# Performance work log

Hardware: AMD Instinct MI355X
Metric: run time of the kernel (lower is better)

## Reference

```python
import jax, jax.numpy as jnp
import numpy as np

N = 100000
E = 1600000
D = 128


def setup_inputs() -> dict:
    key = jax.random.key(0)
    ks = jax.random.split(key, 6)
    x = jax.random.normal(ks[0], (N, D), dtype=jnp.float32)
    edge_row = jax.random.randint(ks[1], (E,), 0, N)
    edge_col = jax.random.randint(ks[2], (E,), 0, N)
    edge_val = jax.random.uniform(ks[3], (E,), dtype=jnp.float32)
    # Kaiming-ish init for the MLP weights
    W1 = jax.random.normal(ks[4], (D, D), dtype=jnp.float32) * (1.0 / np.sqrt(D))
    W2 = jax.random.normal(ks[5], (D, D), dtype=jnp.float32) * (1.0 / np.sqrt(D))
    b1 = jnp.zeros((D,), dtype=jnp.float32)
    b2 = jnp.zeros((D,), dtype=jnp.float32)
    eps = jnp.zeros((1,), dtype=jnp.float32)  # GIN eps, init 0
    bias = jnp.zeros((D,), dtype=jnp.float32)
    return {"x": x, "edge_row": edge_row, "edge_col": edge_col, "edge_val": edge_val,
            "W1": W1, "b1": b1, "W2": W2, "b2": b2, "eps": eps, "bias": bias}


def reference(x, edge_row, edge_col, edge_val, W1, b1, W2, b2, eps, bias):
    # sparse adj @ x : out[i] = sum_{edges (i,j)} val * x[j]
    agg = jax.ops.segment_sum(edge_val[:, None] * x[edge_col], edge_row, num_segments=N)
    h = (1.0 + eps) * x + agg                     # eps-scaled residual, [N, D]
    h = jax.nn.relu(h @ W1 + b1)                  # MLP layer 1
    h = jax.nn.relu(h @ W2 + b2)                  # MLP layer 2
    out = jax.nn.relu(h + bias)                   # bias + final relu
    return out
```

## Files before the change

kernel.cpp:

```cpp
#include <hip/hip_runtime.h>
#include <stdint.h>


static constexpr int NN = 100000;
static constexpr int NE = 1600000;
static constexpr int NB = 391;
static constexpr int EPB = 4096;
static constexpr int PB = (NE + EPB - 1) / EPB;
static constexpr int CVB = 3125;
static constexpr int SCAP = 6144;

typedef float f32x4 __attribute__((ext_vector_type(4)));
typedef short s16x8 __attribute__((ext_vector_type(8)));

__device__ __forceinline__ uint16_t f2bf(float f) {
  uint32_t u = __float_as_uint(f);
  u += 0x7fffu + ((u >> 16) & 1u);
  return (uint16_t)(u >> 16);
}
__device__ __forceinline__ float2 bf2f(uint32_t w) {
  float2 r;
  r.x = __uint_as_float(w << 16);
  r.y = __uint_as_float(w & 0xffff0000u);
  return r;
}

__device__ __forceinline__ int block_scan_inc(int v, int* wsum, int tid) {
  __syncthreads();
  int lane = tid & 63, wv = tid >> 6;
  #pragma unroll
  for (int off = 1; off < 64; off <<= 1) {
    int t = __shfl_up(v, off, 64);
    if (lane >= off) v += t;
  }
  if (lane == 63) wsum[wv] = v;
  __syncthreads();
  if (wv == 0) {
    int s = (lane < 16) ? wsum[lane] : 0;
    #pragma unroll
    for (int off = 1; off < 16; off <<= 1) {
      int t = __shfl_up(s, off, 64);
      if (lane >= off) s += t;
    }
    if (lane < 16) wsum[lane] = s;
  }
  __syncthreads();
  if (wv > 0) v += wsum[wv - 1];
  return v;
}

__global__ __launch_bounds__(1024) void k_pcvt(const float* __restrict__ x,
                                               uint32_t* __restrict__ xb,
                                               const int* __restrict__ erow,
                                               const int* __restrict__ ecol,
                                               const float* __restrict__ eval,
                                               int2* __restrict__ part,
                                               int* __restrict__ runstart) {
  int t = threadIdx.x;
  if (blockIdx.x >= PB) {
    int i = (blockIdx.x - PB) * 1024 + t;
    float4 v = ((const float4*)x)[i];
    uint2 o;
    o.x = (uint32_t)f2bf(v.x) | ((uint32_t)f2bf(v.y) << 16);
    o.y = (uint32_t)f2bf(v.z) | ((uint32_t)f2bf(v.w) << 16);
    ((uint2*)xb)[i] = o;
    return;
  }
  __shared__ int hist[NB];
  __shared__ int cur[NB];
  __shared__ int wsum[16];
  __shared__ int2 stage[EPB];
  int base = blockIdx.x * EPB;
  int cnt = min(EPB, NE - base);

  if (t < NB) hist[t] = 0;
  __syncthreads();

  int pb[4], pk[4], pv[4];
  #pragma unroll
  for (int j = 0; j < 4; ++j) {
    int i = t + j * 1024;
    pb[j] = -1;
    if (i < cnt) {
      int e = base + i;
      int r = erow[e];
      int b = r >> 8;
      pb[j] = b;
      pk[j] = ecol[e] | ((r & 255) << 17);
      pv[j] = __float_as_int(eval[e]);
      atomicAdd(&hist[b], 1);
    }
  }
  __syncthreads();

  int hv = (t < NB) ? hist[t] : 0;
  int inc = block_scan_inc(hv, wsum, t);
  if (t < NB) {
    int st = inc - hv;
    cur[t] = st;
    runstart[blockIdx.x * (NB + 1) + t] = st;
  }
  if (t == 0) runstart[blockIdx.x * (NB + 1) + NB] = cnt;
  __syncthreads();

  #pragma unroll
  for (int j = 0; j < 4; ++j) {
    if (pb[j] >= 0) {
      int off = atomicAdd(&cur[pb[j]], 1);
      stage[off] = int2{pk[j], pv[j]};
    }
  }
  __syncthreads();

  for (int i = t; i < cnt; i += 1024) part[base + i] = stage[i];
}

__global__ __launch_bounds__(1024) void k_aux(const int* __restrict__ runstart,
                                              int* __restrict__ bbase,
                                              int2* __restrict__ es_pad,
                                              const float* __restrict__ W1,
                                              const float* __restrict__ W2,
                                              uint16_t* __restrict__ wtg) {
  int t = threadIdx.x;
  if (blockIdx.x > 0) {
    int base = (blockIdx.x - 1) * 4096;
    #pragma unroll
    for (int j = 0; j < 4; ++j) {
      int idx = base + j * 1024 + t;
      int l = idx >> 14, r = idx & 16383;
      int n = r >> 7, k = r & 127;
      const float* W = l ? W2 : W1;
      wtg[idx] = f2bf(W[k * 128 + n]);
    }
    return;
  }
  __shared__ int psum[2][512];
  __shared__ int wsum[16];
  int g = t >> 9, c = t & 511;
  int acc = 0;
  if (c < NB) {
    for (int p = g; p < PB; p += 2)
      acc += runstart[p * (NB + 1) + c + 1] - runstart[p * (NB + 1) + c];
  }
  psum[g][c] = acc;
  __syncthreads();
  int v = (t < NB) ? psum[0][t] + psum[1][t] : 0;
  int inc = block_scan_inc(v, wsum, t);
  if (t < NB) bbase[t] = inc - v;
  if (t < 16) es_pad[t] = int2{0, 0};
}

__global__ __launch_bounds__(1024) void k_bucket(const int2* __restrict__ part,
                                                 const int* __restrict__ runstart,
                                                 const int* __restrict__ bbase,
                                                 int2* __restrict__ es,
                                                 int* __restrict__ rowptr) {
  __shared__ int cum[PB + 1];
  __shared__ int rbas[PB];
  __shared__ int hist[256];
  __shared__ int rps[256];
  __shared__ int cur[256];
  __shared__ int wsum[16];
  __shared__ int2 stage[SCAP];
  int b = blockIdx.x, t = threadIdx.x;
  int base_out = bbase[b];

  int len = 0;
  if (t < PB) {
    int rs = runstart[t * (NB + 1) + b];
    int re = runstart[t * (NB + 1) + b + 1];
    len = re - rs;
    rbas[t] = t * EPB + rs;
  }
  int inc1 = block_scan_inc(len, wsum, t);
  int mystart = inc1 - len;
  if (t == 1023) cum[PB] = inc1;
  if (t < 256) hist[t] = 0;
  __syncthreads();

  if (t < PB) {
    int rb = rbas[t];
    for (int i = 0; i < len; ++i) {
      int d = mystart + i;
      if (d < SCAP) stage[d] = part[rb + i];
    }
  }
  __syncthreads();

  int total = min(cum[PB], SCAP);

  for (int i = t; i < total; i += 1024)
    atomicAdd(&hist[stage[i].x >> 17], 1);
  __syncthreads();

  int hv = (t < 256) ? hist[t] : 0;
  int inc2 = block_scan_inc(hv, wsum, t);
  if (t < 256) {
    int ex = inc2 - hv;
    rps[t] = ex;
    cur[t] = ex;
  }
  __syncthreads();

  if (t < 256) {
    int row = b * 256 + t;
    if (row <= NN) rowptr[row] = base_out + rps[t];
  }

  for (int i = t; i < total; i += 1024) {
    int2 ev = stage[i];
    int rib = ev.x >> 17;
    int off = atomicAdd(&cur[rib], 1);
    es[base_out + off] = int2{ev.x & 0x1FFFF, ev.y};
  }
}

__global__ __launch_bounds__(256) void k_agg(const uint32_t* __restrict__ xb,
                                             const int2* __restrict__ es,
                                             const int* __restrict__ rowptr,
                                             const float* __restrict__ eps,
                                             uint32_t* __restrict__ hb) {
  int wid = (blockIdx.x * 256 + threadIdx.x) >> 6;
  int wave = __builtin_amdgcn_readfirstlane(wid);
  int lane = threadIdx.x & 63;
  float e = 1.0f + eps[0];
  float2 h = bf2f(xb[(size_t)wave * 64 + lane]);
  h.x *= e; h.y *= e;
  int beg = __builtin_amdgcn_readfirstlane(rowptr[wave]);
  int end = __builtin_amdgcn_readfirstlane(rowptr[wave + 1]);
  for (int k = beg; k < end; k += 8) {
    int scol[8]; float sval[8];
    #pragma unroll
    for (int j = 0; j < 8; ++j) {
      int2 ev = es[k + j];
      scol[j] = __builtin_amdgcn_readfirstlane(ev.x);
      int vb = __builtin_amdgcn_readfirstlane(ev.y);
      sval[j] = (k + j < end) ? __int_as_float(vb) : 0.0f;
    }
    uint32_t xw[8];
    #pragma unroll
    for (int j = 0; j < 8; ++j)
      xw[j] = xb[((size_t)scol[j] << 6) + lane];
    #pragma unroll
    for (int j = 0; j < 8; ++j) {
      float2 xv = bf2f(xw[j]);
      h.x = fmaf(sval[j], xv.x, h.x);
      h.y = fmaf(sval[j], xv.y, h.y);
    }
  }
  hb[(size_t)wave * 64 + lane] = (uint32_t)f2bf(h.x) | ((uint32_t)f2bf(h.y) << 16);
}

__global__ __launch_bounds__(256, 2) void k_mlp(const uint16_t* __restrict__ A,
                                                const uint16_t* __restrict__ wtg,
                                                const float* __restrict__ b1,
                                                const float* __restrict__ b2,
                                                const float* __restrict__ bias,
                                                float* __restrict__ out, int nrows) {
  __shared__ uint16_t wt[128 * 136];
  __shared__ uint16_t h1[128 * 136];
  int tid = threadIdx.x;

  const uint4* wsrc = (const uint4*)wtg;
  #pragma unroll
  for (int it = 0; it < 8; ++it) {
    int idx = tid + it * 256;
    int n = idx >> 4, kq = idx & 15;
    *(uint4*)&wt[n * 136 + kq * 8] = wsrc[idx];
  }
  __syncthreads();

  int wv = tid >> 6, l = tid & 63;
  int m16 = l & 15, qg = l >> 4;
  int r0 = blockIdx.x * 128 + wv * 32;

  int arow[2];
  #pragma unroll
  for (int mt = 0; mt < 2; ++mt) {
    int r = r0 + mt * 16 + m16;
    arow[mt] = (r < nrows) ? r : (nrows - 1);
  }

  f32x4 acc[2][8];
  #pragma unroll
  for (int mt = 0; mt < 2; ++mt)
    #pragma unroll
    for (int n0 = 0; n0 < 8; ++n0) acc[mt][n0] = f32x4{0.f, 0.f, 0.f, 0.f};

  #pragma unroll
  for (int k0 = 0; k0 < 128; k0 += 32) {
    s16x8 a[2];
    #pragma unroll
    for (int mt = 0; mt < 2; ++mt)
      a[mt] = *(const s16x8*)(A + (size_t)arow[mt] * 128 + k0 + qg * 8);
    #pragma unroll
    for (int n0 = 0; n0 < 8; ++n0) {
      s16x8 bfr = *(const s16x8*)(&wt[(n0 * 16 + m16) * 136 + k0 + qg * 8]);
      #pragma unroll
      for (int mt = 0; mt < 2; ++mt)
        acc[mt][n0] = __builtin_amdgcn_mfma_f32_16x16x32_bf16(a[mt], bfr, acc[mt][n0], 0, 0, 0);
    }
  }

  #pragma unroll
  for (int mt = 0; mt < 2; ++mt) {
    #pragma unroll
    for (int n0 = 0; n0 < 8; ++n0) {
      int col = n0 * 16 + m16;
      float bb = b1[col];
      #pragma unroll
      for (int j = 0; j < 4; ++j) {
        int lr = wv * 32 + mt * 16 + qg * 4 + j;
        h1[lr * 136 + col] = f2bf(fmaxf(acc[mt][n0][j] + bb, 0.0f));
      }
    }
  }
  __syncthreads();

  #pragma unroll
  for (int it = 0; it < 8; ++it) {
    int idx = tid + it * 256;
    int n = idx >> 4, kq = idx & 15;
    *(uint4*)&wt[n * 136 + kq * 8] = wsrc[2048 + idx];
  }
  #pragma unroll
  for (int mt = 0; mt < 2; ++mt)
    #pragma unroll
    for (int n0 = 0; n0 < 8; ++n0) acc[mt][n0] = f32x4{0.f, 0.f, 0.f, 0.f};
  __syncthreads();

  #pragma unroll
  for (int k0 = 0; k0 < 128; k0 += 32) {
    s16x8 a[2];
    #pragma unroll
    for (int mt = 0; mt < 2; ++mt)
      a[mt] = *(const s16x8*)(&h1[(wv * 32 + mt * 16 + m16) * 136 + k0 + qg * 8]);
    #pragma unroll
    for (int n0 = 0; n0 < 8; ++n0) {
      s16x8 bfr = *(const s16x8*)(&wt[(n0 * 16 + m16) * 136 + k0 + qg * 8]);
      #pragma unroll
      for (int mt = 0; mt < 2; ++mt)
        acc[mt][n0] = __builtin_amdgcn_mfma_f32_16x16x32_bf16(a[mt], bfr, acc[mt][n0], 0, 0, 0);
    }
  }

  #pragma unroll
  for (int mt = 0; mt < 2; ++mt) {
    #pragma unroll
    for (int n0 = 0; n0 < 8; ++n0) {
      int col = n0 * 16 + m16;
      float bb = b2[col];
      float b3 = bias[col];
      #pragma unroll
      for (int j = 0; j < 4; ++j) {
        int row = r0 + mt * 16 + qg * 4 + j;
        if (row < nrows) {
          float v = fmaxf(fmaxf(acc[mt][n0][j] + bb, 0.0f) + b3, 0.0f);
          out[(size_t)row * 128 + col] = v;
        }
      }
    }
  }
}

extern "C" void kernel_launch(void* const* d_in, const int* in_sizes, int n_in,
                              void* d_out, int out_size, void* d_ws, size_t ws_size,
                              hipStream_t stream) {
  const float* x    = (const float*)d_in[0];
  const int*   erow = (const int*)d_in[1];
  const int*   ecol = (const int*)d_in[2];
  const float* eval = (const float*)d_in[3];
  const float* W1   = (const float*)d_in[4];
  const float* b1   = (const float*)d_in[5];
  const float* W2   = (const float*)d_in[6];
  const float* b2   = (const float*)d_in[7];
  const float* eps  = (const float*)d_in[8];
  const float* bias = (const float*)d_in[9];

  char* w = (char*)d_ws;
  size_t off = 0;
  auto take = [&](size_t bytes) -> void* {
    void* p = w + off;
    off = (off + bytes + 255) & ~(size_t)255;
    return p;
  };
  uint32_t* xb     = (uint32_t*)take((size_t)NN * 64 * 4);
  uint32_t* hb     = (uint32_t*)take((size_t)NN * 64 * 4);
  int2*     part   = (int2*)hb;
  int2*     es     = (int2*)take((size_t)(NE + 16) * 8);
  int*      rowptr = (int*)take((size_t)(NN + 1) * 4);
  int*      runst  = (int*)take((size_t)PB * (NB + 1) * 4);
  int*      bbase  = (int*)take((size_t)(NB + 1) * 4);
  uint16_t* wtg    = (uint16_t*)take(32768 * 2);
  (void)ws_size;

  k_pcvt<<<PB + CVB, 1024, 0, stream>>>(x, xb, erow, ecol, eval, part, runst);
  k_aux<<<9, 1024, 0, stream>>>(runst, bbase, es + NE, W1, W2, wtg);
  k_bucket<<<NB, 1024, 0, stream>>>(part, runst, bbase, es, rowptr);
  k_agg<<<(NN + 3) / 4, 256, 0, stream>>>(xb, es, rowptr, eps, hb);
  k_mlp<<<(NN + 127) / 128, 256, 0, stream>>>((const uint16_t*)hb, wtg, b1, b2,
                                              bias, (float*)d_out, NN);
}
```

Baseline: 269.3 us.

## Prefetch edge chunks in aggregation and parallelize bucket staging across wave lanes

The aggregation kernel now loads the next eight edge entries while it gathers and accumulates the current chunk, so edge-index loads overlap the feature gathers. These prefetches rely on the padded tail of the edge array. In the bucket kernel, each run of edges is now copied into shared staging by a whole wave, with lanes striding through it, instead of by one thread in a serial loop. The aggregation launch is also split into two half-range launches, which adds one extra launch.

```diff
diff --git a/kernel.cpp b/kernel.cpp
--- a/kernel.cpp
+++ b/kernel.cpp
@@ -155,12 +155,14 @@
                                                  const int* __restrict__ bbase,
                                                  int2* __restrict__ es,
                                                  int* __restrict__ rowptr) {
-  __shared__ int cum[PB + 1];
   __shared__ int rbas[PB];
+  __shared__ int cst[PB];
+  __shared__ int rlen[PB];
   __shared__ int hist[256];
   __shared__ int rps[256];
   __shared__ int cur[256];
   __shared__ int wsum[16];
+  __shared__ int tot;
   __shared__ int2 stage[SCAP];
   int b = blockIdx.x, t = threadIdx.x;
   int base_out = bbase[b];
@@ -171,23 +173,23 @@
     int re = runstart[t * (NB + 1) + b + 1];
     len = re - rs;
     rbas[t] = t * EPB + rs;
+    rlen[t] = len;
   }
   int inc1 = block_scan_inc(len, wsum, t);
-  int mystart = inc1 - len;
-  if (t == 1023) cum[PB] = inc1;
+  if (t < PB) cst[t] = inc1 - len;
+  if (t == 1023) tot = inc1;
   if (t < 256) hist[t] = 0;
   __syncthreads();
 
-  if (t < PB) {
-    int rb = rbas[t];
-    for (int i = 0; i < len; ++i) {
-      int d = mystart + i;
-      if (d < SCAP) stage[d] = part[rb + i];
-    }
-  }
-  __syncthreads();
-
-  int total = min(cum[PB], SCAP);
+  int total = min(tot, SCAP);
+
+  int lane = t & 63, wv = t >> 6;
+  for (int r = wv; r < PB; r += 16) {
+    int st = cst[r], ln = rlen[r], rb = rbas[r];
+    if (st + ln > SCAP) ln = max(0, SCAP - st);
+    for (int i = lane; i < ln; i += 64) stage[st + i] = part[rb + i];
+  }
+  __syncthreads();
 
   for (int i = t; i < total; i += 1024)
     atomicAdd(&hist[stage[i].x >> 17], 1);
@@ -219,8 +221,8 @@
                                              const int2* __restrict__ es,
                                              const int* __restrict__ rowptr,
                                              const float* __restrict__ eps,
-                                             uint32_t* __restrict__ hb) {
-  int wid = (blockIdx.x * 256 + threadIdx.x) >> 6;
+                                             uint32_t* __restrict__ hb, int row0) {
+  int wid = row0 + ((blockIdx.x * 256 + threadIdx.x) >> 6);
   int wave = __builtin_amdgcn_readfirstlane(wid);
   int lane = threadIdx.x & 63;
   float e = 1.0f + eps[0];
@@ -228,25 +230,32 @@
   h.x *= e; h.y *= e;
   int beg = __builtin_amdgcn_readfirstlane(rowptr[wave]);
   int end = __builtin_amdgcn_readfirstlane(rowptr[wave + 1]);
+
+  int2 curc[8];
+  #pragma unroll
+  for (int j = 0; j < 8; ++j) curc[j] = es[beg + j];
+
   for (int k = beg; k < end; k += 8) {
-    int scol[8]; float sval[8];
+    float sv[8];
+    uint32_t xw[8];
     #pragma unroll
     for (int j = 0; j < 8; ++j) {
-      int2 ev = es[k + j];
-      scol[j] = __builtin_amdgcn_readfirstlane(ev.x);
-      int vb = __builtin_amdgcn_readfirstlane(ev.y);
-      sval[j] = (k + j < end) ? __int_as_float(vb) : 0.0f;
-    }
-    uint32_t xw[8];
-    #pragma unroll
-    for (int j = 0; j < 8; ++j)
-      xw[j] = xb[((size_t)scol[j] << 6) + lane];
+      int sc = __builtin_amdgcn_readfirstlane(curc[j].x);
+      int vb = __builtin_amdgcn_readfirstlane(curc[j].y);
+      sv[j] = (k + j < end) ? __int_as_float(vb) : 0.0f;
+      xw[j] = xb[((size_t)sc << 6) + lane];
+    }
+    int2 nxt[8];
+    #pragma unroll
+    for (int j = 0; j < 8; ++j) nxt[j] = es[k + 8 + j];
     #pragma unroll
     for (int j = 0; j < 8; ++j) {
       float2 xv = bf2f(xw[j]);
-      h.x = fmaf(sval[j], xv.x, h.x);
-      h.y = fmaf(sval[j], xv.y, h.y);
-    }
+      h.x = fmaf(sv[j], xv.x, h.x);
+      h.y = fmaf(sv[j], xv.y, h.y);
+    }
+    #pragma unroll
+    for (int j = 0; j < 8; ++j) curc[j] = nxt[j];
   }
   hb[(size_t)wave * 64 + lane] = (uint32_t)f2bf(h.x) | ((uint32_t)f2bf(h.y) << 16);
 }
@@ -397,7 +406,8 @@
   k_pcvt<<<PB + CVB, 1024, 0, stream>>>(x, xb, erow, ecol, eval, part, runst);
   k_aux<<<9, 1024, 0, stream>>>(runst, bbase, es + NE, W1, W2, wtg);
   k_bucket<<<NB, 1024, 0, stream>>>(part, runst, bbase, es, rowptr);
-  k_agg<<<(NN + 3) / 4, 256, 0, stream>>>(xb, es, rowptr, eps, hb);
+  k_agg<<<(NN / 2) / 4, 256, 0, stream>>>(xb, es, rowptr, eps, hb, 0);
+  k_agg<<<(NN / 2) / 4, 256, 0, stream>>>(xb, es, rowptr, eps, hb, NN / 2);
   k_mlp<<<(NN + 127) / 128, 256, 0, stream>>>((const uint16_t*)hb, wtg, b1, b2,
                                               bias, (float*)d_out, NN);
 }
```

Result: no change. 271.6 us (+0.8%).
